# Performance work log

Measured on AMD Instinct MI355X. Metric: run time of the kernel, lower is better.

The kernel has to match this reference:

```python
import jax, jax.numpy as jnp
import numpy as np

T, IN, M, C, OUT = 8192, 1024, 64, 16, 1024  # time, input, trace, context, output


def _ln(x, eps=1e-5):
    mu = jnp.mean(x, axis=-1, keepdims=True)
    var = jnp.var(x, axis=-1, keepdims=True)
    return (x - mu) * jax.lax.rsqrt(var + eps)


def _mish(x):
    return x * jnp.tanh(jax.nn.softplus(x))


def setup_inputs() -> dict:
    key = jax.random.key(0)
    ks = jax.random.split(key, 8)

    def w(k, o, i):
        return (jax.random.normal(k, (o, i), jnp.float32) / np.sqrt(i).astype(np.float32))

    return {
        "x": jax.random.normal(ks[0], (T, IN), jnp.float32),
        "state0": jnp.zeros((1, M, C), jnp.float32),  # real part of complex zero init
        "start": jax.random.uniform(ks[1], (T,)) < 0.002,  # sparse episode resets
        "next_done": jnp.zeros((T,), bool),  # unused by the sequential-equivalent math
        "a": jnp.linspace(1e-6, 0.5, M, dtype=jnp.float32),  # ffa.init decay
        "bf": (2.0 * jnp.pi / jnp.linspace(1.0, 1024.0, C)).astype(jnp.float32),  # ffa.init freqs
        "pre_w": w(ks[2], M, IN), "pre_b": jnp.zeros((M,), jnp.float32),
        "skip_w": w(ks[3], OUT, IN), "skip_b": jnp.zeros((OUT,), jnp.float32),
        "mix_w1": w(ks[4], M * C, 2 * M * C), "mix_b1": jnp.zeros((M * C,), jnp.float32),
        "mix_w2": w(ks[5], M * C, M * C), "mix_b2": jnp.zeros((M * C,), jnp.float32),
        "mix_w3": w(ks[6], OUT, M * C), "mix_b3": jnp.zeros((OUT,), jnp.float32),
    }


def _forward(x, state0, start, a, bf, pre_w, pre_b, skip_w, skip_b,
             mix_w1, mix_b1, mix_w2, mix_b2, mix_w3, mix_b3):
    Tn = x.shape[0]
    # pre = softplus(Linear(LayerNorm(x)))  -> [T, M]
    pre = jax.nn.softplus(_ln(x) @ pre_w.T + pre_b)
    # one-step FFA decay gamma[m,c] = exp(-|a_m| + i*b_c)
    la = jnp.broadcast_to(-jnp.abs(a)[:, None], (a.shape[0], bf.shape[0]))
    lb = jnp.broadcast_to(bf[None, :], la.shape)
    gamma = jnp.exp(jax.lax.complex(la, lb))  # [M, C] complex64
    # reset monoid: s_t = A_t * s_{t-1} + b_t,  A_t = 0 where episode starts
    A = jnp.where(start[:, None, None], jnp.zeros((), gamma.dtype), gamma[None])  # [T,M,C]
    b_el = jnp.broadcast_to(pre[:, :, None].astype(gamma.dtype), A.shape)  # [T,M,C]
    s_init = state0.astype(gamma.dtype)  # [1, M, C]
    b_el = b_el.at[0].add(A[0] * s_init[0])  # fold carried state into first element

    def combine(lhs, rhs):
        Al, bl = lhs
        Ar, br = rhs
        return Ar * Al, Ar * bl + br

    _, s = jax.lax.associative_scan(combine, (A, b_el))  # s: [T, M, C] states at every t

    s_flat = s.reshape(Tn, M * C)
    # global (all-element) complex mean / real std normalization, as in the source
    scaled = (s_flat - jnp.mean(s_flat)) / (1e-6 + jnp.std(s_flat))
    z = jnp.concatenate([scaled.real, scaled.imag], axis=-1)  # [T, 2*M*C]
    z = _mish(z @ mix_w1.T + mix_b1)
    z = _mish(z @ mix_w2.T + mix_b2)
    z = z @ mix_w3.T + mix_b3  # [T, OUT]
    out = _ln(z + (x @ skip_w.T + skip_b))
    return out, s[-1:]


def reference(x, state0, start, next_done, a, bf, pre_w, pre_b, skip_w, skip_b,
              mix_w1, mix_b1, mix_w2, mix_b2, mix_w3, mix_b3):
    return _forward(x, state0, start, a, bf, pre_w, pre_b, skip_w, skip_b,
                    mix_w1, mix_b1, mix_w2, mix_b2, mix_w3, mix_b3)
```

## Files before the change

kernel.cpp:

```cpp
#include <hip/hip_runtime.h>
#include <hip/hip_bf16.h>

#define T_    8192
#define INDIM 1024
#define MTR   64
#define CCTX  16
#define MC    1024
#define NOUT  1024
#define CHUNK 64
#define NCH   128

using bf16x8 = __attribute__((ext_vector_type(8))) short;
using f32x4  = __attribute__((ext_vector_type(4))) float;

__device__ __forceinline__ unsigned short f2bf(float f) {
  unsigned int u = __builtin_bit_cast(unsigned int, f);
  u += 0x7fffu + ((u >> 16) & 1u);
  return (unsigned short)(u >> 16);
}
__device__ __forceinline__ float bf2f(unsigned short u) {
  return __builtin_bit_cast(float, (unsigned int)u << 16);
}

__device__ __forceinline__ float mish_f(float v) {
  float u = __expf(v);
  float w = u * (u + 2.f);
  return (v > 20.f) ? v : v * __fdividef(w, w + 2.f);
}

typedef __attribute__((address_space(1))) void gas_void;
typedef __attribute__((address_space(3))) void las_void;

__device__ __forceinline__ void gload_lds16(const void* g, void* l) {
  __builtin_amdgcn_global_load_lds((gas_void*)g, (las_void*)l, 16, 0, 0);
}

__device__ __forceinline__ float2 block_sum2(float s, float ss, float* sbuf) {
#pragma unroll
  for (int off = 32; off > 0; off >>= 1) {
    s  += __shfl_down(s, off);
    ss += __shfl_down(ss, off);
  }
  if ((threadIdx.x & 63) == 0) {
    sbuf[(threadIdx.x >> 6) * 2]     = s;
    sbuf[(threadIdx.x >> 6) * 2 + 1] = ss;
  }
  __syncthreads();
  return make_float2(sbuf[0] + sbuf[2] + sbuf[4] + sbuf[6],
                     sbuf[1] + sbuf[3] + sbuf[5] + sbuf[7]);
}

__global__ __launch_bounds__(256) void prep_k(const float* __restrict__ w1, const float* __restrict__ w2,
                                              const float* __restrict__ w3, const float* __restrict__ sw,
                                              const float* __restrict__ x,
                                              unsigned short* __restrict__ o1, unsigned short* __restrict__ o2,
                                              unsigned short* __restrict__ o3, unsigned short* __restrict__ o4,
                                              float* __restrict__ wre, float* __restrict__ wim,
                                              float2* __restrict__ rowstat, unsigned short* __restrict__ xb) {
  __shared__ float sbuf[8];
  const int b = blockIdx.x;
  if (b < 5120) {
    long i = ((long)b * 256 + threadIdx.x) * 4;
    const float* src; unsigned short* dst; long off;
    if (i < 2097152)      { src = w1; dst = o1; off = i; }
    else if (i < 3145728) { src = w2; dst = o2; off = i - 2097152; }
    else if (i < 4194304) { src = w3; dst = o3; off = i - 3145728; }
    else if (i < 5242880) { src = sw; dst = o4; off = i - 4194304; }
    else return;
    float4 v = *(const float4*)(src + off);
    ushort4 o = { f2bf(v.x), f2bf(v.y), f2bf(v.z), f2bf(v.w) };
    *(ushort4*)(dst + off) = o;
  } else if (b < 6144) {
    const long row = b - 5120;
    const float4* r4 = (const float4*)(w1 + row * 2048);
    float4 a = r4[threadIdx.x];
    float4 c = r4[256 + threadIdx.x];
    float2 t = block_sum2(a.x + a.y + a.z + a.w, c.x + c.y + c.z + c.w, sbuf);
    if (threadIdx.x == 0) { wre[row] = t.x; wim[row] = t.y; }
  } else {
    const long row = b - 6144;
    float4 v = ((const float4*)(x + (row << 10)))[threadIdx.x];
    ushort4 c = { f2bf(v.x), f2bf(v.y), f2bf(v.z), f2bf(v.w) };
    ((ushort4*)(xb + (row << 10)))[threadIdx.x] = c;
    float2 t = block_sum2(v.x + v.y + v.z + v.w,
                          v.x * v.x + v.y * v.y + v.z * v.z + v.w * v.w, sbuf);
    float mean = t.x * (1.f / 1024.f);
    float var  = t.y * (1.f / 1024.f) - mean * mean;
    float rstd = rsqrtf(var + 1e-5f);
    if (threadIdx.x == 0) rowstat[row] = make_float2(mean, rstd);
  }
}

__global__ __launch_bounds__(256) void ln_out1b_k(const unsigned short* __restrict__ p, float* __restrict__ out) {
  __shared__ float sbuf[8];
  const long row = blockIdx.x;
  ushort4 u4 = ((const ushort4*)(p + (row << 10)))[threadIdx.x];
  float4 v = { bf2f(u4.x), bf2f(u4.y), bf2f(u4.z), bf2f(u4.w) };
  float2 t = block_sum2(v.x + v.y + v.z + v.w,
                        v.x * v.x + v.y * v.y + v.z * v.z + v.w * v.w, sbuf);
  float mean = t.x * (1.f / 1024.f);
  float var  = t.y * (1.f / 1024.f) - mean * mean;
  float rstd = rsqrtf(var + 1e-5f);
  float4 o = { (v.x - mean) * rstd, (v.y - mean) * rstd,
               (v.z - mean) * rstd, (v.w - mean) * rstd };
  ((float4*)(out + (row << 10)))[threadIdx.x] = o;
}

__global__ __launch_bounds__(256) void pre_part_k(const float* __restrict__ x,
                                                  const float2* __restrict__ rowstat,
                                                  const float* __restrict__ pw,
                                                  float* __restrict__ part) {
  const int lane = threadIdx.x & 63;
  const int wvu  = __builtin_amdgcn_readfirstlane(threadIdx.x >> 6);
  const int kc   = blockIdx.y;
  const int r0   = (blockIdx.x * 4 + wvu) * 32;

  const float* wrow = pw + (long)lane * 1024 + kc * 128;
  float wreg[128];
#pragma unroll
  for (int j = 0; j < 32; ++j)
    *(float4*)&wreg[j * 4] = ((const float4*)wrow)[j];
  float swsum = 0.f;
#pragma unroll
  for (int j = 0; j < 128; ++j) swsum += wreg[j];

  float* po = part + ((long)kc * T_ + r0) * 64 + lane;
  const float* xbase = x + (long)r0 * 1024 + kc * 128;

  for (int i = 0; i < 32; i += 2) {
    const float4* xr0 = (const float4*)(xbase + (long)i * 1024);
    const float4* xr1 = (const float4*)(xbase + (long)(i + 1) * 1024);
    float a0 = 0.f, a1 = 0.f, a2 = 0.f, a3 = 0.f;
    float b0 = 0.f, b1 = 0.f, b2 = 0.f, b3 = 0.f;
#pragma unroll
    for (int j = 0; j < 32; j += 4) {
      float4 xa0 = xr0[j],     xa1 = xr0[j + 1], xa2 = xr0[j + 2], xa3 = xr0[j + 3];
      float4 xb0 = xr1[j],     xb1 = xr1[j + 1], xb2 = xr1[j + 2], xb3 = xr1[j + 3];
      a0 += wreg[4*j+0]*xa0.x  + wreg[4*j+1]*xa0.y  + wreg[4*j+2]*xa0.z  + wreg[4*j+3]*xa0.w;
      a1 += wreg[4*j+4]*xa1.x  + wreg[4*j+5]*xa1.y  + wreg[4*j+6]*xa1.z  + wreg[4*j+7]*xa1.w;
      a2 += wreg[4*j+8]*xa2.x  + wreg[4*j+9]*xa2.y  + wreg[4*j+10]*xa2.z + wreg[4*j+11]*xa2.w;
      a3 += wreg[4*j+12]*xa3.x + wreg[4*j+13]*xa3.y + wreg[4*j+14]*xa3.z + wreg[4*j+15]*xa3.w;
      b0 += wreg[4*j+0]*xb0.x  + wreg[4*j+1]*xb0.y  + wreg[4*j+2]*xb0.z  + wreg[4*j+3]*xb0.w;
      b1 += wreg[4*j+4]*xb1.x  + wreg[4*j+5]*xb1.y  + wreg[4*j+6]*xb1.z  + wreg[4*j+7]*xb1.w;
      b2 += wreg[4*j+8]*xb2.x  + wreg[4*j+9]*xb2.y  + wreg[4*j+10]*xb2.z + wreg[4*j+11]*xb2.w;
      b3 += wreg[4*j+12]*xb3.x + wreg[4*j+13]*xb3.y + wreg[4*j+14]*xb3.z + wreg[4*j+15]*xb3.w;
    }
    float2 s0 = rowstat[r0 + i];
    float2 s1 = rowstat[r0 + i + 1];
    po[(long)i * 64]       = s0.y * ((a0 + a1) + (a2 + a3)) - s0.x * s0.y * swsum;
    po[(long)(i + 1) * 64] = s1.y * ((b0 + b1) + (b2 + b3)) - s1.x * s1.y * swsum;
  }
}

__global__ __launch_bounds__(256) void scan_p1f(const float* __restrict__ part,
                                                const float* __restrict__ pb,
                                                const int* __restrict__ start,
                                                const float* __restrict__ a, const float* __restrict__ bfr,
                                                float* __restrict__ pre,
                                                double2* __restrict__ chA, double2* __restrict__ chB) {
  __shared__ float ps[64][16];
  const int j = blockIdx.x;
  const int yq = blockIdx.y;
  const int t0 = j * CHUNK;
#pragma unroll
  for (int r = 0; r < 4; ++r) {
    int p = threadIdx.x + 256 * r;
    int tt = p >> 4, mm = p & 15;
    int m = yq * 16 + mm;
    long idx = (long)(t0 + tt) * 64 + m;
    float s = 0.f;
#pragma unroll
    for (int kc = 0; kc < 8; ++kc)
      s += part[(long)kc * T_ * 64 + idx];
    float v = s + pb[m];
    float sp = fmaxf(v, 0.f) + log1pf(expf(-fabsf(v)));
    pre[idx] = sp;
    ps[tt][mm] = sp;
  }
  __syncthreads();
  int ch = yq * 256 + threadIdx.x;
  int m = ch >> 4, c = ch & 15;
  int mm = threadIdx.x >> 4;
  double dec = exp(-fabs((double)a[m]));
  double th = (double)bfr[c];
  double gre = dec * cos(th), gim = dec * sin(th);
  double pr = 1.0, pi = 0.0, sr = 0.0, si = 0.0;
  for (int t = 0; t < CHUNK; ++t) {
    double b = (double)ps[t][mm];
    if (start[t0 + t]) {
      pr = 0.0; pi = 0.0; sr = b; si = 0.0;
    } else {
      double nsr = gre * sr - gim * si + b;
      si = gre * si + gim * sr; sr = nsr;
      double npr = gre * pr - gim * pi;
      pi = gre * pi + gim * pr; pr = npr;
    }
  }
  chA[j * MC + ch] = make_double2(pr, pi);
  chB[j * MC + ch] = make_double2(sr, si);
}

__global__ __launch_bounds__(64) void scan_p2(const double2* __restrict__ chA, const double2* __restrict__ chB,
                                              const float* __restrict__ state0,
                                              double2* __restrict__ carry, double* __restrict__ red,
                                              float* __restrict__ out_tail, int fmt) {
  if (blockIdx.x == 0 && threadIdx.x < 4) red[threadIdx.x] = 0.0;
  int ch = blockIdx.x * 64 + threadIdx.x;
  double cr = (double)state0[ch], ci = 0.0;
  for (int j = 0; j < NCH; ++j) {
    carry[j * MC + ch] = make_double2(cr, ci);
    double2 A = chA[j * MC + ch];
    double2 B = chB[j * MC + ch];
    double ncr = A.x * cr - A.y * ci + B.x;
    ci = A.x * ci + A.y * cr + B.y;
    cr = ncr;
  }
  if (fmt == 1024) {
    out_tail[ch] = (float)cr;
  } else {
    out_tail[2 * ch]     = (float)cr;
    out_tail[2 * ch + 1] = (float)ci;
  }
}

__global__ __launch_bounds__(256) void scan_p3(const float* __restrict__ pre, const int* __restrict__ start,
                                               const float* __restrict__ a, const float* __restrict__ bfr,
                                               const double2* __restrict__ carry,
                                               double* __restrict__ red,
                                               unsigned short* __restrict__ z) {
  __shared__ double sbuf[12];
  int ch = blockIdx.y * 256 + threadIdx.x;
  int m = ch >> 4, c = ch & 15;
  double dec = exp(-fabs((double)a[m]));
  double th = (double)bfr[c];
  double gre = dec * cos(th), gim = dec * sin(th);
  int j = blockIdx.x;
  int t0 = j * CHUNK;
  double2 cin = carry[j * MC + ch];
  double sr = cin.x, si = cin.y;
  double aR = 0.0, aI = 0.0, aS = 0.0;
  for (int t = t0; t < t0 + CHUNK; ++t) {
    double b = (double)pre[(long)t * 64 + m];
    if (start[t]) { sr = b; si = 0.0; }
    else {
      double nsr = gre * sr - gim * si + b;
      si = gre * si + gim * sr; sr = nsr;
    }
    z[(long)t * 2048 + ch]        = f2bf((float)sr);
    z[(long)t * 2048 + 1024 + ch] = f2bf((float)si);
    aR += sr; aI += si; aS += sr * sr + si * si;
  }
#pragma unroll
  for (int off = 32; off > 0; off >>= 1) {
    aR += __shfl_down(aR, off); aI += __shfl_down(aI, off); aS += __shfl_down(aS, off);
  }
  if ((threadIdx.x & 63) == 0) {
    int w = threadIdx.x >> 6;
    sbuf[w * 3] = aR; sbuf[w * 3 + 1] = aI; sbuf[w * 3 + 2] = aS;
  }
  __syncthreads();
  if (threadIdx.x == 0) {
    atomicAdd(&red[0], sbuf[0] + sbuf[3] + sbuf[6] + sbuf[9]);
    atomicAdd(&red[1], sbuf[1] + sbuf[4] + sbuf[7] + sbuf[10]);
    atomicAdd(&red[2], sbuf[2] + sbuf[5] + sbuf[8] + sbuf[11]);
  }
}

#define TSZ (128 * 32)
template<int EP>
__device__ __forceinline__ void gemm128_core(const unsigned short* __restrict__ A,
                                             const unsigned short* __restrict__ B,
                                             const float* __restrict__ bias,
                                             const unsigned short* __restrict__ addb,
                                             const double* __restrict__ red,
                                             const float* __restrict__ wre,
                                             const float* __restrict__ wim,
                                             void* __restrict__ Cout,
                                             int bx, int by, int N_, int K_,
                                             unsigned short* lA, unsigned short* lB) {
  const int tid = threadIdx.x;
  const int lane = tid & 63;
  const int wv = tid >> 6;
  const int wr = wv >> 1, wc = wv & 1;
  const long brow = (long)bx * 128;
  const long bcol = (long)by * 128;

  f32x4 acc[4][4];
#pragma unroll
  for (int i = 0; i < 4; i++)
#pragma unroll
    for (int j = 0; j < 4; j++)
      acc[i][j] = f32x4{0.f, 0.f, 0.f, 0.f};

  const int c0 = tid, c1 = tid + 256;
  const long ar0 = brow + (c0 >> 2), ar1 = brow + (c1 >> 2);
  const long br0 = bcol + (c0 >> 2), br1 = bcol + (c1 >> 2);
  const int ko0 = (((c0 & 3) ^ ((c0 >> 3) & 3)) * 8);
  const int ko1 = (((c1 & 3) ^ ((c1 >> 3) & 3)) * 8);
  const int r15 = lane & 15;
  const int swzq = (((lane >> 4) ^ ((r15 >> 1) & 3)) * 8);

  const int nt = K_ >> 5;

#define STAGE(ti, bu)                                                      \
  do {                                                                     \
    gload_lds16(A + ar0 * K_ + (ti) * 32 + ko0, lA + (bu) * TSZ + c0 * 8); \
    gload_lds16(A + ar1 * K_ + (ti) * 32 + ko1, lA + (bu) * TSZ + c1 * 8); \
    gload_lds16(B + br0 * K_ + (ti) * 32 + ko0, lB + (bu) * TSZ + c0 * 8); \
    gload_lds16(B + br1 * K_ + (ti) * 32 + ko1, lB + (bu) * TSZ + c1 * 8); \
  } while (0)

  STAGE(0, 0);
  STAGE(1, 1);

  for (int i = 0; i < nt; ++i) {
    if (i + 2 < nt) {
      STAGE(i + 2, (i + 2) & 3);
      asm volatile("s_waitcnt vmcnt(8)" ::: "memory");
    } else if (i + 1 < nt) {
      asm volatile("s_waitcnt vmcnt(4)" ::: "memory");
    } else {
      asm volatile("s_waitcnt vmcnt(0)" ::: "memory");
    }
    __builtin_amdgcn_sched_barrier(0);
    __builtin_amdgcn_s_barrier();
    __builtin_amdgcn_sched_barrier(0);

    const unsigned short* bA = lA + (i & 3) * TSZ;
    const unsigned short* bB = lB + (i & 3) * TSZ;
    bf16x8 af[4], bv[4];
#pragma unroll
    for (int mi = 0; mi < 4; mi++)
      af[mi] = *(const bf16x8*)&bA[(wr * 64 + mi * 16 + r15) * 32 + swzq];
#pragma unroll
    for (int nj = 0; nj < 4; nj++)
      bv[nj] = *(const bf16x8*)&bB[(wc * 64 + nj * 16 + r15) * 32 + swzq];
    __builtin_amdgcn_s_setprio(1);
#pragma unroll
    for (int mi = 0; mi < 4; mi++)
#pragma unroll
      for (int nj = 0; nj < 4; nj++)
        acc[mi][nj] = __builtin_amdgcn_mfma_f32_16x16x32_bf16(af[mi], bv[nj], acc[mi][nj], 0, 0, 0);
    __builtin_amdgcn_s_setprio(0);
  }
#undef STAGE

  float cre = 0.f, cim = 0.f, inv = 1.f;
  if (EP == 4) {
    const double n = (double)T_ * (double)MC;
    double mre = red[0] / n, mim = red[1] / n;
    double var = red[2] / n - mre * mre - mim * mim;
    double sd = sqrt(var > 0.0 ? var : 0.0);
    cre = (float)mre; cim = (float)mim; inv = (float)(1.0 / (1e-6 + sd));
  }

  const int rq = (lane >> 4) * 4;
#pragma unroll
  for (int nj = 0; nj < 4; nj++) {
    const long col = bcol + wc * 64 + nj * 16 + r15;
    const float bs = bias[col];
    float wrc = 0.f, wic = 0.f;
    if (EP == 4) { wrc = wre[col]; wic = wim[col]; }
#pragma unroll
    for (int mi = 0; mi < 4; mi++) {
#pragma unroll
      for (int r = 0; r < 4; r++) {
        const long row = brow + wr * 64 + mi * 16 + rq + r;
        float va = acc[mi][nj][r];
        if (EP == 1) {
          ((unsigned short*)Cout)[row * N_ + col] = f2bf(va + bs);
        } else if (EP == 3) {
          float v = va + bs + bf2f(addb[row * N_ + col]);
          ((unsigned short*)Cout)[row * N_ + col] = f2bf(v);
        } else if (EP == 4) {
          float v = (va - cre * wrc - cim * wic) * inv + bs;
          ((unsigned short*)Cout)[row * N_ + col] = f2bf(mish_f(v));
        } else {
          ((unsigned short*)Cout)[row * N_ + col] = f2bf(mish_f(va + bs));
        }
      }
    }
  }
}

template<int EP>
__global__ __launch_bounds__(256) void gemm128_k(const unsigned short* __restrict__ A,
                                                 const unsigned short* __restrict__ B,
                                                 const float* __restrict__ bias,
                                                 const unsigned short* __restrict__ addb,
                                                 void* __restrict__ Cout, int N_, int K_) {
  __shared__ __align__(16) unsigned short lA[4 * TSZ];
  __shared__ __align__(16) unsigned short lB[4 * TSZ];
  gemm128_core<EP>(A, B, bias, addb, nullptr, nullptr, nullptr, Cout,
                   blockIdx.x, blockIdx.y, N_, K_, lA, lB);
}

__global__ __launch_bounds__(256) void gemm_dual128(const unsigned short* __restrict__ A1,
                                                    const unsigned short* __restrict__ B1,
                                                    const float* __restrict__ bias1,
                                                    unsigned short* __restrict__ C1, int K1,
                                                    const double* __restrict__ red,
                                                    const float* __restrict__ wre,
                                                    const float* __restrict__ wim,
                                                    const unsigned short* __restrict__ A2,
                                                    const unsigned short* __restrict__ B2,
                                                    const float* __restrict__ bias2,
                                                    unsigned short* __restrict__ C2, int K2) {
  __shared__ __align__(16) unsigned short lA[4 * TSZ];
  __shared__ __align__(16) unsigned short lB[4 * TSZ];
  int b = blockIdx.x;
  if (b < 512) {
    gemm128_core<4>(A1, B1, bias1, nullptr, red, wre, wim, C1, b & 63, b >> 6, 1024, K1, lA, lB);
  } else {
    b -= 512;
    gemm128_core<1>(A2, B2, bias2, nullptr, nullptr, nullptr, nullptr, C2, b & 63, b >> 6, 1024, K2, lA, lB);
  }
}

extern "C" void kernel_launch(void* const* d_in, const int* in_sizes, int n_in,
                              void* d_out, int out_size, void* d_ws, size_t ws_size,
                              hipStream_t stream) {
  (void)in_sizes; (void)n_in; (void)ws_size;
  const float* x      = (const float*)d_in[0];
  const float* state0 = (const float*)d_in[1];
  const int*   start  = (const int*)d_in[2];
  const float* a      = (const float*)d_in[4];
  const float* bfr    = (const float*)d_in[5];
  const float* pre_w  = (const float*)d_in[6];
  const float* pre_b  = (const float*)d_in[7];
  const float* skip_w = (const float*)d_in[8];
  const float* skip_b = (const float*)d_in[9];
  const float* w1     = (const float*)d_in[10];
  const float* b1     = (const float*)d_in[11];
  const float* w2     = (const float*)d_in[12];
  const float* b2     = (const float*)d_in[13];
  const float* w3     = (const float*)d_in[14];
  const float* b3     = (const float*)d_in[15];

  char* ws = (char*)d_ws;
  const size_t MB = 1u << 20;
  unsigned short* skipb = (unsigned short*)(ws + 0);
  float*          part  = (float*)(ws + 16 * MB);
  unsigned short* h3b   = (unsigned short*)(ws + 48 * MB);
  unsigned short* z     = (unsigned short*)(ws + 64 * MB);
  unsigned short* xb    = (unsigned short*)(ws + 96 * MB);
  unsigned short* h2    = (unsigned short*)(ws + 96 * MB);
  unsigned short* h1    = (unsigned short*)(ws + 112 * MB);
  unsigned short* wb1   = (unsigned short*)(ws + 128 * MB);
  unsigned short* wb2   = (unsigned short*)(ws + 132 * MB);
  unsigned short* wb3   = (unsigned short*)(ws + 134 * MB);
  unsigned short* skwb  = (unsigned short*)(ws + 136 * MB);
  float*          pre   = (float*)(ws + 138 * MB);
  double2*        chA   = (double2*)(ws + 140 * MB);
  double2*        chB   = (double2*)(ws + 142 * MB);
  double2*        carry = (double2*)(ws + 144 * MB);
  double*         red   = (double*)(ws + 146 * MB);
  float2*         rowst = (float2*)(ws + 147 * MB);
  float*          wre   = (float*)(ws + 147 * MB + 65536);
  float*          wim   = (float*)(ws + 147 * MB + 65536 + 4096);

  prep_k<<<14336, 256, 0, stream>>>(w1, w2, w3, skip_w, x,
                                    wb1, wb2, wb3, skwb, wre, wim, rowst, xb);

  pre_part_k<<<dim3(64, 8), 256, 0, stream>>>(x, rowst, pre_w, part);

  int tail_elems = out_size - T_ * NOUT;
  float* out_tail = (float*)d_out + (long)T_ * NOUT;
  scan_p1f<<<dim3(NCH, 4), 256, 0, stream>>>(part, pre_b, start, a, bfr, pre, chA, chB);
  scan_p2<<<16, 64, 0, stream>>>(chA, chB, state0, carry, red, out_tail, tail_elems);
  scan_p3<<<dim3(NCH, 4), 256, 0, stream>>>(pre, start, a, bfr, carry, red, z);

  gemm_dual128<<<1024, 256, 0, stream>>>(z, wb1, b1, h1, 2048, red, wre, wim,
                                         xb, skwb, skip_b, skipb, 1024);
  gemm128_k<2><<<dim3(64, 8), 256, 0, stream>>>(h1, wb2, b2, nullptr, h2, 1024, 1024);
  gemm128_k<3><<<dim3(64, 8), 256, 0, stream>>>(h2, wb3, b3, skipb, h3b, 1024, 1024);

  ln_out1b_k<<<8192, 256, 0, stream>>>(h3b, (float*)d_out);
}
```

Baseline: 257.0 us.

## Use 256x256 tiles with 512 threads for the dual first-layer/skip GEMM

Replaces the 128x128-tile dual GEMM, which ran 1024 blocks of 256 threads, with a new 256x256-tile core using 8 waves and a 4-deep LDS ring buffer. Each launch is now 256 blocks of 512 threads. Larger tiles raise arithmetic intensity and cut global/L2 traffic per FLOP for the mix_w1 and skip GEMMs. In exchange, 256 blocks only about fill the 256 CUs with one block each, LDS use is much higher, and each wave holds 32 accumulators, which risks register pressure and lower occupancy.

New measurement: 261.1 us. Within noise of the previous version (+1.6%).

```diff
diff --git a/kernel.cpp b/kernel.cpp
--- a/kernel.cpp
+++ b/kernel.cpp
@@ -395,7 +395,118 @@
                    blockIdx.x, blockIdx.y, N_, K_, lA, lB);
 }
 
-__global__ __launch_bounds__(256) void gemm_dual128(const unsigned short* __restrict__ A1,
+#define TSZ256 (256 * 32)
+template<int EP>
+__device__ __forceinline__ void gemm256_core(const unsigned short* __restrict__ A,
+                                             const unsigned short* __restrict__ B,
+                                             const float* __restrict__ bias,
+                                             const double* __restrict__ red,
+                                             const float* __restrict__ wre,
+                                             const float* __restrict__ wim,
+                                             void* __restrict__ Cout,
+                                             int bx, int by, int N_, int K_,
+                                             unsigned short* lA, unsigned short* lB) {
+  const int tid = threadIdx.x;
+  const int lane = tid & 63;
+  const int wv = tid >> 6;
+  const int wr = wv >> 2, wc = wv & 3;
+  const long brow = (long)bx * 256;
+  const long bcol = (long)by * 256;
+
+  f32x4 acc[8][4];
+#pragma unroll
+  for (int i = 0; i < 8; i++)
+#pragma unroll
+    for (int j = 0; j < 4; j++)
+      acc[i][j] = f32x4{0.f, 0.f, 0.f, 0.f};
+
+  const int c0 = tid, c1 = tid + 512;
+  const long ar0 = brow + (c0 >> 2), ar1 = brow + (c1 >> 2);
+  const long br0 = bcol + (c0 >> 2), br1 = bcol + (c1 >> 2);
+  const int ko0 = (((c0 & 3) ^ ((c0 >> 3) & 3)) * 8);
+  const int ko1 = (((c1 & 3) ^ ((c1 >> 3) & 3)) * 8);
+  const int r15 = lane & 15;
+  const int swzq = (((lane >> 4) ^ ((r15 >> 1) & 3)) * 8);
+
+  const int nt = K_ >> 5;
+
+#define STAGE6(ti, bu)                                                        \
+  do {                                                                        \
+    gload_lds16(A + ar0 * K_ + (ti) * 32 + ko0, lA + (bu) * TSZ256 + c0 * 8); \
+    gload_lds16(A + ar1 * K_ + (ti) * 32 + ko1, lA + (bu) * TSZ256 + c1 * 8); \
+    gload_lds16(B + br0 * K_ + (ti) * 32 + ko0, lB + (bu) * TSZ256 + c0 * 8); \
+    gload_lds16(B + br1 * K_ + (ti) * 32 + ko1, lB + (bu) * TSZ256 + c1 * 8); \
+  } while (0)
+
+  STAGE6(0, 0);
+  STAGE6(1, 1);
+
+  for (int i = 0; i < nt; ++i) {
+    if (i + 2 < nt) {
+      STAGE6(i + 2, (i + 2) & 3);
+      asm volatile("s_waitcnt vmcnt(8)" ::: "memory");
+    } else if (i + 1 < nt) {
+      asm volatile("s_waitcnt vmcnt(4)" ::: "memory");
+    } else {
+      asm volatile("s_waitcnt vmcnt(0)" ::: "memory");
+    }
+    __builtin_amdgcn_sched_barrier(0);
+    __builtin_amdgcn_s_barrier();
+    __builtin_amdgcn_sched_barrier(0);
+
+    const unsigned short* bA = lA + (i & 3) * TSZ256;
+    const unsigned short* bB = lB + (i & 3) * TSZ256;
+    bf16x8 af[8], bv[4];
+#pragma unroll
+    for (int mi = 0; mi < 8; mi++)
+      af[mi] = *(const bf16x8*)&bA[(wr * 128 + mi * 16 + r15) * 32 + swzq];
+#pragma unroll
+    for (int nj = 0; nj < 4; nj++)
+      bv[nj] = *(const bf16x8*)&bB[(wc * 64 + nj * 16 + r15) * 32 + swzq];
+    __builtin_amdgcn_s_setprio(1);
+#pragma unroll
+    for (int mi = 0; mi < 8; mi++)
+#pragma unroll
+      for (int nj = 0; nj < 4; nj++)
+        acc[mi][nj] = __builtin_amdgcn_mfma_f32_16x16x32_bf16(af[mi], bv[nj], acc[mi][nj], 0, 0, 0);
+    __builtin_amdgcn_s_setprio(0);
+  }
+#undef STAGE6
+
+  float cre = 0.f, cim = 0.f, inv = 1.f;
+  if (EP == 4) {
+    const double n = (double)T_ * (double)MC;
+    double mre = red[0] / n, mim = red[1] / n;
+    double var = red[2] / n - mre * mre - mim * mim;
+    double sd = sqrt(var > 0.0 ? var : 0.0);
+    cre = (float)mre; cim = (float)mim; inv = (float)(1.0 / (1e-6 + sd));
+  }
+
+  const int rq = (lane >> 4) * 4;
+#pragma unroll
+  for (int nj = 0; nj < 4; nj++) {
+    const long col = bcol + wc * 64 + nj * 16 + r15;
+    const float bs = bias[col];
+    float wrc = 0.f, wic = 0.f;
+    if (EP == 4) { wrc = wre[col]; wic = wim[col]; }
+#pragma unroll
+    for (int mi = 0; mi < 8; mi++) {
+#pragma unroll
+      for (int r = 0; r < 4; r++) {
+        const long row = brow + wr * 128 + mi * 16 + rq + r;
+        float va = acc[mi][nj][r];
+        if (EP == 4) {
+          float v = (va - cre * wrc - cim * wic) * inv + bs;
+          ((unsigned short*)Cout)[row * N_ + col] = f2bf(mish_f(v));
+        } else {
+          ((unsigned short*)Cout)[row * N_ + col] = f2bf(va + bs);
+        }
+      }
+    }
+  }
+}
+
+__global__ __launch_bounds__(512) void gemm_dual256(const unsigned short* __restrict__ A1,
                                                     const unsigned short* __restrict__ B1,
                                                     const float* __restrict__ bias1,
                                                     unsigned short* __restrict__ C1, int K1,
@@ -406,14 +517,14 @@
                                                     const unsigned short* __restrict__ B2,
                                                     const float* __restrict__ bias2,
                                                     unsigned short* __restrict__ C2, int K2) {
-  __shared__ __align__(16) unsigned short lA[4 * TSZ];
-  __shared__ __align__(16) unsigned short lB[4 * TSZ];
+  __shared__ __align__(16) unsigned short lA[4 * TSZ256];
+  __shared__ __align__(16) unsigned short lB[4 * TSZ256];
   int b = blockIdx.x;
-  if (b < 512) {
-    gemm128_core<4>(A1, B1, bias1, nullptr, red, wre, wim, C1, b & 63, b >> 6, 1024, K1, lA, lB);
+  if (b < 128) {
+    gemm256_core<4>(A1, B1, bias1, red, wre, wim, C1, b & 31, b >> 5, 1024, K1, lA, lB);
   } else {
-    b -= 512;
-    gemm128_core<1>(A2, B2, bias2, nullptr, nullptr, nullptr, nullptr, C2, b & 63, b >> 6, 1024, K2, lA, lB);
+    b -= 128;
+    gemm256_core<1>(A2, B2, bias2, nullptr, nullptr, nullptr, C2, b & 31, b >> 5, 1024, K2, lA, lB);
   }
 }
 
@@ -470,8 +581,8 @@
   scan_p2<<<16, 64, 0, stream>>>(chA, chB, state0, carry, red, out_tail, tail_elems);
   scan_p3<<<dim3(NCH, 4), 256, 0, stream>>>(pre, start, a, bfr, carry, red, z);
 
-  gemm_dual128<<<1024, 256, 0, stream>>>(z, wb1, b1, h1, 2048, red, wre, wim,
-                                         xb, skwb, skip_b, skipb, 1024);
+  gemm_dual256<<<256, 512, 0, stream>>>(z, wb1, b1, h1, 2048, red, wre, wim,
+                                        xb, skwb, skip_b, skipb, 1024);
   gemm128_k<2><<<dim3(64, 8), 256, 0, stream>>>(h1, wb2, b2, nullptr, h2, 1024, 1024);
   gemm128_k<3><<<dim3(64, 8), 256, 0, stream>>>(h2, wb3, b3, skipb, h3b, 1024, 1024);
 
```

## Fuse three-phase chunked scan into one cooperative kernel with grid syncs

Applied to the files above, without the earlier changes.

Replaces the three scan launches (chunk-local scan, serial carry propagation, chunk re-scan with output) with a single cooperative kernel that uses grid-wide syncs between phases. The softplus pre-activations stay in shared memory across phases, so the intermediate pre buffer is no longer written and re-read, and two kernel launch gaps go away. It risks cooperative-launch overhead and the cost of grid barriers, and keeps the old three-kernel path as a fallback if the cooperative launch fails.

Measured after the change: 363.2 us. 41.3% more time.

```diff
diff --git a/kernel.cpp b/kernel.cpp
--- a/kernel.cpp
+++ b/kernel.cpp
@@ -1,5 +1,7 @@
 #include <hip/hip_runtime.h>
 #include <hip/hip_bf16.h>
+#include <hip/hip_cooperative_groups.h>
+namespace cg = cooperative_groups;
 
 #define T_    8192
 #define INDIM 1024
@@ -152,6 +154,115 @@
   }
 }
 
+__global__ __launch_bounds__(256) void scan_coop(const float* __restrict__ part,
+                                                 const float* __restrict__ pb,
+                                                 const int* __restrict__ start,
+                                                 const float* __restrict__ a, const float* __restrict__ bfr,
+                                                 const float* __restrict__ state0,
+                                                 double2* __restrict__ chA, double2* __restrict__ chB,
+                                                 double2* __restrict__ carry, double* __restrict__ red,
+                                                 float* __restrict__ out_tail, int fmt,
+                                                 unsigned short* __restrict__ z) {
+  __shared__ float ps[64][16];
+  __shared__ double sbuf[12];
+  const int bid = blockIdx.x;
+  const int j = bid & 127;
+  const int yq = bid >> 7;
+  const int t0 = j * CHUNK;
+
+#pragma unroll
+  for (int r = 0; r < 4; ++r) {
+    int p = threadIdx.x + 256 * r;
+    int tt = p >> 4, mm = p & 15;
+    int m = yq * 16 + mm;
+    long idx = (long)(t0 + tt) * 64 + m;
+    float s = 0.f;
+#pragma unroll
+    for (int kc = 0; kc < 8; ++kc)
+      s += part[(long)kc * T_ * 64 + idx];
+    float v = s + pb[m];
+    float sp = fmaxf(v, 0.f) + log1pf(expf(-fabsf(v)));
+    ps[tt][mm] = sp;
+  }
+  if (bid == 0 && threadIdx.x < 4) red[threadIdx.x] = 0.0;
+  __syncthreads();
+
+  const int ch = yq * 256 + threadIdx.x;
+  const int m = ch >> 4, c = ch & 15;
+  const int mm = threadIdx.x >> 4;
+  const double dec = exp(-fabs((double)a[m]));
+  const double th = (double)bfr[c];
+  const double gre = dec * cos(th), gim = dec * sin(th);
+  {
+    double pr = 1.0, pi = 0.0, sr = 0.0, si = 0.0;
+    for (int t = 0; t < CHUNK; ++t) {
+      double b = (double)ps[t][mm];
+      if (start[t0 + t]) {
+        pr = 0.0; pi = 0.0; sr = b; si = 0.0;
+      } else {
+        double nsr = gre * sr - gim * si + b;
+        si = gre * si + gim * sr; sr = nsr;
+        double npr = gre * pr - gim * pi;
+        pi = gre * pi + gim * pr; pr = npr;
+      }
+    }
+    chA[j * MC + ch] = make_double2(pr, pi);
+    chB[j * MC + ch] = make_double2(sr, si);
+  }
+
+  cg::this_grid().sync();
+
+  if (bid < 16 && threadIdx.x < 64) {
+    int ch2 = bid * 64 + threadIdx.x;
+    double cr = (double)state0[ch2], ci = 0.0;
+    for (int jj = 0; jj < NCH; ++jj) {
+      carry[jj * MC + ch2] = make_double2(cr, ci);
+      double2 A = chA[jj * MC + ch2];
+      double2 Bv = chB[jj * MC + ch2];
+      double ncr = A.x * cr - A.y * ci + Bv.x;
+      ci = A.x * ci + A.y * cr + Bv.y;
+      cr = ncr;
+    }
+    if (fmt == 1024) {
+      out_tail[ch2] = (float)cr;
+    } else {
+      out_tail[2 * ch2]     = (float)cr;
+      out_tail[2 * ch2 + 1] = (float)ci;
+    }
+  }
+
+  cg::this_grid().sync();
+
+  double2 cin = carry[j * MC + ch];
+  double sr = cin.x, si = cin.y;
+  double aR = 0.0, aI = 0.0, aS = 0.0;
+  for (int t = 0; t < CHUNK; ++t) {
+    double b = (double)ps[t][mm];
+    if (start[t0 + t]) { sr = b; si = 0.0; }
+    else {
+      double nsr = gre * sr - gim * si + b;
+      si = gre * si + gim * sr; sr = nsr;
+    }
+    z[(long)(t0 + t) * 2048 + ch]        = f2bf((float)sr);
+    z[(long)(t0 + t) * 2048 + 1024 + ch] = f2bf((float)si);
+    aR += sr; aI += si; aS += sr * sr + si * si;
+  }
+#pragma unroll
+  for (int off = 32; off > 0; off >>= 1) {
+    aR += __shfl_down(aR, off); aI += __shfl_down(aI, off); aS += __shfl_down(aS, off);
+  }
+  if ((threadIdx.x & 63) == 0) {
+    int w = threadIdx.x >> 6;
+    sbuf[w * 3] = aR; sbuf[w * 3 + 1] = aI; sbuf[w * 3 + 2] = aS;
+  }
+  __syncthreads();
+  if (threadIdx.x == 0) {
+    atomicAdd(&red[0], sbuf[0] + sbuf[3] + sbuf[6] + sbuf[9]);
+    atomicAdd(&red[1], sbuf[1] + sbuf[4] + sbuf[7] + sbuf[10]);
+    atomicAdd(&red[2], sbuf[2] + sbuf[5] + sbuf[8] + sbuf[11]);
+  }
+}
+
 __global__ __launch_bounds__(256) void scan_p1f(const float* __restrict__ part,
                                                 const float* __restrict__ pb,
                                                 const int* __restrict__ start,
@@ -466,9 +577,21 @@
 
   int tail_elems = out_size - T_ * NOUT;
   float* out_tail = (float*)d_out + (long)T_ * NOUT;
-  scan_p1f<<<dim3(NCH, 4), 256, 0, stream>>>(part, pre_b, start, a, bfr, pre, chA, chB);
-  scan_p2<<<16, 64, 0, stream>>>(chA, chB, state0, carry, red, out_tail, tail_elems);
-  scan_p3<<<dim3(NCH, 4), 256, 0, stream>>>(pre, start, a, bfr, carry, red, z);
+  {
+    const float* pbp = pre_b;  const int* stp = start;
+    const float* ap = a;       const float* bp = bfr;
+    const float* s0p = state0;
+    void* cargs[] = { (void*)&part, (void*)&pbp, (void*)&stp, (void*)&ap, (void*)&bp,
+                      (void*)&s0p, (void*)&chA, (void*)&chB, (void*)&carry, (void*)&red,
+                      (void*)&out_tail, (void*)&tail_elems, (void*)&z };
+    hipError_t cerr = hipLaunchCooperativeKernel((void*)scan_coop, dim3(512), dim3(256),
+                                                 cargs, 0, stream);
+    if (cerr != hipSuccess) {
+      scan_p1f<<<dim3(NCH, 4), 256, 0, stream>>>(part, pre_b, start, a, bfr, pre, chA, chB);
+      scan_p2<<<16, 64, 0, stream>>>(chA, chB, state0, carry, red, out_tail, tail_elems);
+      scan_p3<<<dim3(NCH, 4), 256, 0, stream>>>(pre, start, a, bfr, carry, red, z);
+    }
+  }
 
   gemm_dual128<<<1024, 256, 0, stream>>>(z, wb1, b1, h1, 2048, red, wre, wim,
                                          xb, skwb, skip_b, skipb, 1024);
```
